# Performance work log

Hardware: AMD Instinct MI355X
Metric: run time of the kernel (lower is better)

The kernel has to match this reference:

```python
import jax, jax.numpy as jnp
import numpy as np

N_NODES = 1500
E = 48000
IN = 128
OUT = 32
HEADS = 4
EDIM = 16


def setup_inputs() -> dict:
    key = jax.random.key(0)
    ks = jax.random.split(key, 16)
    rn = lambda k, shape, s=0.1: jax.random.normal(k, shape, dtype=jnp.float32) * s
    return {
        "x": jax.random.normal(ks[0], (N_NODES, IN), dtype=jnp.float32),
        "edges": jax.random.randint(ks[1], (2, E), 0, N_NODES),
        "edge_feature": jax.random.normal(ks[2], (E, EDIM), dtype=jnp.float32),
        "W1": rn(ks[3], (IN, HEADS * OUT)),
        "att_src1": rn(ks[4], (HEADS, OUT)),
        "att_dst1": rn(ks[5], (HEADS, OUT)),
        "We": rn(ks[6], (EDIM, HEADS * OUT)),
        "att_e": rn(ks[7], (HEADS, OUT)),
        "b1": jnp.zeros((OUT,), jnp.float32),
        "W2": rn(ks[8], (OUT, HEADS * OUT)),
        "att_src2": rn(ks[9], (HEADS, OUT)),
        "att_dst2": rn(ks[10], (HEADS, OUT)),
        "b2": jnp.zeros((OUT,), jnp.float32),
        "fc1_w": rn(ks[11], (2 * OUT, 32)),
        "fc1_b": jnp.zeros((32,), jnp.float32),
        "fc2_w": rn(ks[12], (32, 2)),
        "fc2_b": jnp.zeros((2,), jnp.float32),
    }


def _gat(h, src, dst, n, a_src, a_dst, bias, extra_alpha=None):
    # h: [n, H, C] projected node features; edges j=src -> i=dst (PyG GATConv)
    alpha = (h * a_src).sum(-1)[src] + (h * a_dst).sum(-1)[dst]  # [Etot, H]
    if extra_alpha is not None:
        alpha = alpha + extra_alpha
    alpha = jax.nn.leaky_relu(alpha, negative_slope=0.2)
    m = jax.ops.segment_max(alpha, dst, num_segments=n)  # per-dst softmax (stable)
    e = jnp.exp(alpha - m[dst])
    s = jax.ops.segment_sum(e, dst, num_segments=n)
    w = e / s[dst]  # every node has a self loop -> denom > 0
    out = jax.ops.segment_sum(w[:, :, None] * h[src], dst, num_segments=n)  # [n, H, C]
    return out.mean(axis=1) + bias  # concat=False -> mean over heads


def reference(x, edges, edge_feature, W1, att_src1, att_dst1, We, att_e, b1,
              W2, att_src2, att_dst2, b2, fc1_w, fc1_b, fc2_w, fc2_b):
    n = x.shape[0]
    src0, dst0 = edges[0], edges[1]
    loop = jnp.arange(n, dtype=src0.dtype)
    src = jnp.concatenate([src0, loop])
    dst = jnp.concatenate([dst0, loop])
    # add_self_loops fill_value='mean': self-loop attr = mean of incoming edge attrs
    cnt = jax.ops.segment_sum(jnp.ones_like(dst0, dtype=jnp.float32), dst0, num_segments=n)
    loop_attr = jax.ops.segment_sum(edge_feature, dst0, num_segments=n) / jnp.maximum(cnt, 1.0)[:, None]
    ea = jnp.concatenate([edge_feature, loop_attr], axis=0)  # [E+n, EDIM]

    H, C = att_src1.shape
    # layer 1: GATConv with edge features
    h1 = (x @ W1).reshape(n, H, C)
    extra = ((ea @ We).reshape(-1, H, C) * att_e).sum(-1)  # [E+n, H]
    x1 = _gat(h1, src, dst, n, att_src1, att_dst1, b1, extra)  # [n, OUT]
    # layer 2: GATConv without edge features
    h2 = (x1 @ W2).reshape(n, H, C)
    x2 = _gat(h2, src, dst, n, att_src2, att_dst2, b2)  # [n, OUT]

    # per-edge gather-concat into a (n^2, 2*OUT) buffer; rows >= E stay zero,
    # exactly as the original Python loop leaves them
    pair = jnp.concatenate([x2[src0], x2[dst0]], axis=1)  # [E, 2*OUT]
    x_edges = jnp.zeros((n * n, 2 * C), dtype=x2.dtype).at[jnp.arange(src0.shape[0])].set(pair)
    hcls = jax.nn.relu(x_edges @ fc1_w + fc1_b)
    return jax.nn.softmax(hcls @ fc2_w + fc2_b, axis=1)
```

## Files before the change

kernel.cpp:

```cpp
#include <hip/hip_runtime.h>
#include <cmath>

#define N_NODES 1500
#define NE 48000
#define ETOT (NE + N_NODES)
#define IN_DIM 128
#define OUT_DIM 32
#define HEADS 4
#define HC 128
#define EDIM 16
#define CH 128

__global__ void k_init(int* deg, int* fillc, float* sumattr) {
    int gid = blockIdx.x * blockDim.x + threadIdx.x;
    if (gid < N_NODES) { deg[gid] = 0; fillc[gid] = 0; }
    if (gid < N_NODES * EDIM) sumattr[gid] = 0.f;
}

__global__ void k_deg_attr(const int* __restrict__ dst, const float* __restrict__ ef,
                           int* deg, float* sumattr) {
    int gid = blockIdx.x * blockDim.x + threadIdx.x;
    if (gid >= NE * EDIM) return;
    int e = gid >> 4, k = gid & 15;
    int d = dst[e];
    atomicAdd(&sumattr[d * EDIM + k], ef[gid]);
    if (k == 0) atomicAdd(&deg[d], 1);
}

__global__ void k_scan(const int* __restrict__ deg, int* __restrict__ off) {
    __shared__ int part[512];
    int t = threadIdx.x;
    int base = t * 3;
    int d0 = (base     < N_NODES) ? deg[base] + 1     : 0;
    int d1 = (base + 1 < N_NODES) ? deg[base + 1] + 1 : 0;
    int d2 = (base + 2 < N_NODES) ? deg[base + 2] + 1 : 0;
    int sum = d0 + d1 + d2;
    part[t] = sum;
    __syncthreads();
    for (int o = 1; o < 512; o <<= 1) {
        int v = (t >= o) ? part[t - o] : 0;
        __syncthreads();
        part[t] += v;
        __syncthreads();
    }
    int excl = part[t] - sum;
    if (base     <= N_NODES) off[base]     = excl;
    if (base + 1 <= N_NODES) off[base + 1] = excl + d0;
    if (base + 2 <= N_NODES) off[base + 2] = excl + d0 + d1;
}

__global__ void k_scatter(const int* __restrict__ src, const int* __restrict__ dst,
                          const int* __restrict__ off, int* fillc,
                          int* __restrict__ csr_src, int* __restrict__ csr_eid) {
    int e = blockIdx.x * blockDim.x + threadIdx.x;
    if (e >= ETOT) return;
    int s, d;
    if (e < NE) { s = src[e]; d = dst[e]; } else { s = d = e - NE; }
    int pos = atomicAdd(&fillc[d], 1);
    int idx = off[d] + pos;
    csr_src[idx] = s;
    csr_eid[idx] = e;
}

__global__ void k_extra(const float* __restrict__ ef, const float* __restrict__ We,
                        const float* __restrict__ att_e, const float* __restrict__ sumattr,
                        const int* __restrict__ deg, float* __restrict__ extra) {
    __shared__ float P[EDIM * HEADS];
    int t = threadIdx.x;
    if (t < EDIM * HEADS) {
        int k = t >> 2, hh = t & 3;
        float a = 0.f;
        #pragma unroll
        for (int c = 0; c < OUT_DIM; ++c)
            a = fmaf(We[k * HC + hh * OUT_DIM + c], att_e[hh * OUT_DIM + c], a);
        P[t] = a;
    }
    __syncthreads();
    int gid = blockIdx.x * blockDim.x + t;
    if (gid >= ETOT * HEADS) return;
    int e = gid >> 2, hh = gid & 3;
    float a = 0.f;
    if (e < NE) {
        #pragma unroll
        for (int k = 0; k < EDIM; ++k) a = fmaf(ef[e * EDIM + k], P[k * 4 + hh], a);
    } else {
        int i = e - NE;
        float inv = 1.0f / fmaxf((float)deg[i], 1.0f);
        #pragma unroll
        for (int k = 0; k < EDIM; ++k) a = fmaf(sumattr[i * EDIM + k] * inv, P[k * 4 + hh], a);
    }
    extra[gid] = a;
}

__global__ void k_proj1(const float* __restrict__ xin, const float* __restrict__ W,
                        const float* __restrict__ a_src, const float* __restrict__ a_dst,
                        float* __restrict__ h, float* __restrict__ asrc, float* __restrict__ adst) {
    __shared__ float xs[4][IN_DIM];
    int i0 = blockIdx.x * 4, t = threadIdx.x;
    #pragma unroll
    for (int r = 0; r < 4; ++r) xs[r][t] = xin[(i0 + r) * IN_DIM + t];
    __syncthreads();
    float acc0 = 0.f, acc1 = 0.f, acc2 = 0.f, acc3 = 0.f;
    for (int k = 0; k < IN_DIM; ++k) {
        float w = W[k * HC + t];
        acc0 = fmaf(xs[0][k], w, acc0);
        acc1 = fmaf(xs[1][k], w, acc1);
        acc2 = fmaf(xs[2][k], w, acc2);
        acc3 = fmaf(xs[3][k], w, acc3);
    }
    float as = a_src[t], ad = a_dst[t];
    int hh = t >> 5, c = t & 31;
    float accs[4] = {acc0, acc1, acc2, acc3};
    #pragma unroll
    for (int r = 0; r < 4; ++r) {
        h[(i0 + r) * HC + t] = accs[r];
        float ps = accs[r] * as, pd = accs[r] * ad;
        #pragma unroll
        for (int o = 16; o >= 1; o >>= 1) {
            ps += __shfl_down(ps, o, 32);
            pd += __shfl_down(pd, o, 32);
        }
        if (c == 0) { asrc[(i0 + r) * 4 + hh] = ps; adst[(i0 + r) * 4 + hh] = pd; }
    }
}

template <int MODE>
__global__ void k_gat(const float* __restrict__ h, const float* __restrict__ asrc,
                      const float* __restrict__ adst, const float* __restrict__ extra,
                      const int* __restrict__ off, const int* __restrict__ csr_src,
                      const int* __restrict__ csr_eid, const float* __restrict__ bias,
                      const float* __restrict__ Wn, const float* __restrict__ a_s2,
                      const float* __restrict__ a_d2,
                      float* __restrict__ h2, float* __restrict__ asrc2,
                      float* __restrict__ adst2, float* __restrict__ uv) {
    __shared__ int   sns[CH];
    __shared__ float sal[CH * HEADS];
    __shared__ float red[HC];
    __shared__ float xrow[OUT_DIM];
    int i = blockIdx.x, t = threadIdx.x;
    int hh = t >> 5, c = t & 31;
    float4 ad4 = *(const float4*)&adst[i * 4];
    int beg = off[i], end = off[i + 1];
    float m = -INFINITY, s = 0.f, acc = 0.f;
    for (int pos = beg; pos < end; pos += CH) {
        int cnt = min(CH, end - pos);
        __syncthreads();
        if (t < cnt) {
            int j = pos + t;
            int sn = csr_src[j];
            sns[t] = sn;
            float4 a4 = *(const float4*)&asrc[sn * 4];
            float ax = a4.x + ad4.x, ay = a4.y + ad4.y, az = a4.z + ad4.z, aw = a4.w + ad4.w;
            if (MODE == 1) {
                float4 e4 = *(const float4*)&extra[csr_eid[j] * 4];
                ax += e4.x; ay += e4.y; az += e4.z; aw += e4.w;
            }
            ax = ax > 0.f ? ax : 0.2f * ax;
            ay = ay > 0.f ? ay : 0.2f * ay;
            az = az > 0.f ? az : 0.2f * az;
            aw = aw > 0.f ? aw : 0.2f * aw;
            *(float4*)&sal[t * 4] = make_float4(ax, ay, az, aw);
        }
        __syncthreads();
        float cm = -INFINITY;
        for (int q = c; q < cnt; q += 32) cm = fmaxf(cm, sal[q * 4 + hh]);
        #pragma unroll
        for (int o = 16; o >= 1; o >>= 1) cm = fmaxf(cm, __shfl_down(cm, o, 32));
        cm = __shfl(cm, 0, 32);
        float mn = fmaxf(m, cm);
        float r = __expf(m - mn);
        float cs = 0.f;
        for (int q = c; q < cnt; q += 32) {
            float w = __expf(sal[q * 4 + hh] - mn);
            sal[q * 4 + hh] = w;
            cs += w;
        }
        #pragma unroll
        for (int o = 16; o >= 1; o >>= 1) cs += __shfl_down(cs, o, 32);
        cs = __shfl(cs, 0, 32);
        s = s * r + cs;
        acc *= r;
        m = mn;
        for (int jj = 0; jj < cnt; ++jj)
            acc = fmaf(sal[jj * 4 + hh], h[sns[jj] * HC + t], acc);
    }
    red[t] = acc / s;
    __syncthreads();
    if (t < OUT_DIM)
        xrow[t] = 0.25f * (red[t] + red[t + 32] + red[t + 64] + red[t + 96]) + bias[t];
    __syncthreads();
    if (MODE == 1) {
        float a2 = 0.f;
        #pragma unroll
        for (int k = 0; k < OUT_DIM; ++k) a2 = fmaf(xrow[k], Wn[k * HC + t], a2);
        h2[i * HC + t] = a2;
        float ps = a2 * a_s2[t], pd = a2 * a_d2[t];
        #pragma unroll
        for (int o = 16; o >= 1; o >>= 1) {
            ps += __shfl_down(ps, o, 32);
            pd += __shfl_down(pd, o, 32);
        }
        if (c == 0) { asrc2[i * 4 + hh] = ps; adst2[i * 4 + hh] = pd; }
    } else {
        if (t < 64) {
            int j = t & 31, ro = (t >> 5) * 32;
            float a2 = 0.f;
            #pragma unroll
            for (int k = 0; k < OUT_DIM; ++k) a2 = fmaf(xrow[k], Wn[(ro + k) * 32 + j], a2);
            uv[i * 64 + t] = a2;
        }
    }
}

__global__ void k_fill(const float* __restrict__ fc1b, const float* __restrict__ fc2w,
                       const float* __restrict__ fc2b, float* __restrict__ out) {
    float l0 = fc2b[0], l1 = fc2b[1];
    #pragma unroll
    for (int j = 0; j < 32; ++j) {
        float a = fmaxf(fc1b[j], 0.f);
        l0 = fmaf(a, fc2w[2 * j], l0);
        l1 = fmaf(a, fc2w[2 * j + 1], l1);
    }
    float mx = fmaxf(l0, l1);
    float e0 = __expf(l0 - mx), e1 = __expf(l1 - mx);
    float inv = 1.f / (e0 + e1);
    float4 q = make_float4(e0 * inv, e1 * inv, e0 * inv, e1 * inv);
    int gid = blockIdx.x * blockDim.x + threadIdx.x;
    const int nfl4 = ((N_NODES * N_NODES - NE) * 2) / 4;
    if (gid < nfl4) ((float4*)(out + NE * 2))[gid] = q;
}

__global__ void k_edge_mlp(const int* __restrict__ src, const int* __restrict__ dst,
                           const float* __restrict__ uv,
                           const float* __restrict__ fc1b,
                           const float* __restrict__ fc2w, const float* __restrict__ fc2b,
                           float* __restrict__ out) {
    __shared__ float b1s[32], w2s[64], b2s[2];
    int t = threadIdx.x;
    if (t < 32) b1s[t] = fc1b[t];
    if (t < 64) w2s[t] = fc2w[t];
    if (t < 2)  b2s[t] = fc2b[t];
    __syncthreads();
    int e = blockIdx.x * 256 + t;
    if (e >= NE) return;
    int si = src[e], di = dst[e];
    const float4* up = (const float4*)&uv[si * 64];
    const float4* vp = (const float4*)&uv[di * 64 + 32];
    float l0 = b2s[0], l1 = b2s[1];
    #pragma unroll
    for (int q = 0; q < 8; ++q) {
        float4 u4 = up[q], v4 = vp[q];
        float a;
        a = fmaxf(u4.x + v4.x + b1s[4*q+0], 0.f); l0 = fmaf(a, w2s[8*q+0], l0); l1 = fmaf(a, w2s[8*q+1], l1);
        a = fmaxf(u4.y + v4.y + b1s[4*q+1], 0.f); l0 = fmaf(a, w2s[8*q+2], l0); l1 = fmaf(a, w2s[8*q+3], l1);
        a = fmaxf(u4.z + v4.z + b1s[4*q+2], 0.f); l0 = fmaf(a, w2s[8*q+4], l0); l1 = fmaf(a, w2s[8*q+5], l1);
        a = fmaxf(u4.w + v4.w + b1s[4*q+3], 0.f); l0 = fmaf(a, w2s[8*q+6], l0); l1 = fmaf(a, w2s[8*q+7], l1);
    }
    float mx = fmaxf(l0, l1);
    float e0 = __expf(l0 - mx), e1 = __expf(l1 - mx);
    float inv = 1.f / (e0 + e1);
    *(float2*)&out[2 * e] = make_float2(e0 * inv, e1 * inv);
}

extern "C" void kernel_launch(void* const* d_in, const int* in_sizes, int n_in,
                              void* d_out, int out_size, void* d_ws, size_t ws_size,
                              hipStream_t stream) {
    (void)in_sizes; (void)n_in; (void)out_size; (void)ws_size;
    const float* x    = (const float*)d_in[0];
    const int*  edges = (const int*)d_in[1];
    const float* ef   = (const float*)d_in[2];
    const float* W1   = (const float*)d_in[3];
    const float* as1  = (const float*)d_in[4];
    const float* ad1  = (const float*)d_in[5];
    const float* We   = (const float*)d_in[6];
    const float* ate  = (const float*)d_in[7];
    const float* b1   = (const float*)d_in[8];
    const float* W2   = (const float*)d_in[9];
    const float* as2  = (const float*)d_in[10];
    const float* ad2  = (const float*)d_in[11];
    const float* b2   = (const float*)d_in[12];
    const float* fc1w = (const float*)d_in[13];
    const float* fc1b = (const float*)d_in[14];
    const float* fc2w = (const float*)d_in[15];
    const float* fc2b = (const float*)d_in[16];
    const int* src = edges;
    const int* dst = edges + NE;
    float* out = (float*)d_out;

    char* w = (char*)d_ws;
    auto alloc = [&](size_t bytes) -> char* {
        char* p = w;
        w += (bytes + 255) & ~(size_t)255;
        return p;
    };
    float* h1      = (float*)alloc((size_t)N_NODES * HC * 4);
    float* asrc1   = (float*)alloc((size_t)N_NODES * HEADS * 4);
    float* adst1   = (float*)alloc((size_t)N_NODES * HEADS * 4);
    float* extra   = (float*)alloc((size_t)ETOT * HEADS * 4);
    float* sumattr = (float*)alloc((size_t)N_NODES * EDIM * 4);
    int*   deg     = (int*)  alloc((size_t)N_NODES * 4);
    int*   off     = (int*)  alloc((size_t)(N_NODES + 1) * 4);
    int*   fillc   = (int*)  alloc((size_t)N_NODES * 4);
    int*   csr_src = (int*)  alloc((size_t)ETOT * 4);
    int*   csr_eid = (int*)  alloc((size_t)ETOT * 4);
    float* h2      = (float*)alloc((size_t)N_NODES * HC * 4);
    float* asrc2   = (float*)alloc((size_t)N_NODES * HEADS * 4);
    float* adst2   = (float*)alloc((size_t)N_NODES * HEADS * 4);
    float* uv      = (float*)alloc((size_t)N_NODES * 64 * 4);

    const int B = 256;
    k_init<<<(N_NODES * EDIM + B - 1) / B, B, 0, stream>>>(deg, fillc, sumattr);
    k_deg_attr<<<(NE * EDIM + B - 1) / B, B, 0, stream>>>(dst, ef, deg, sumattr);
    k_scan<<<1, 512, 0, stream>>>(deg, off);
    k_scatter<<<(ETOT + B - 1) / B, B, 0, stream>>>(src, dst, off, fillc, csr_src, csr_eid);
    k_extra<<<(ETOT * HEADS + B - 1) / B, B, 0, stream>>>(ef, We, ate, sumattr, deg, extra);
    k_proj1<<<N_NODES / 4, HC, 0, stream>>>(x, W1, as1, ad1, h1, asrc1, adst1);
    k_gat<1><<<N_NODES, HC, 0, stream>>>(h1, asrc1, adst1, extra, off, csr_src, csr_eid, b1,
                                         W2, as2, ad2, h2, asrc2, adst2, nullptr);
    k_gat<2><<<N_NODES, HC, 0, stream>>>(h2, asrc2, adst2, nullptr, off, csr_src, csr_eid, b2,
                                         fc1w, nullptr, nullptr, nullptr, nullptr, nullptr, uv);
    k_fill<<<((((N_NODES * N_NODES - NE) * 2) / 4) + B - 1) / B, B, 0, stream>>>(fc1b, fc2w, fc2b, out);
    k_edge_mlp<<<(NE + B - 1) / B, B, 0, stream>>>(src, dst, uv, fc1b, fc2w, fc2b, out);
}
```

Before: 157.9 us.

## Fuse all GAT pipeline stages into one persistent kernel with grid barriers

Ten separate launches (init, degree/attribute accumulation, scan, CSR scatter, edge-attention term, projection, two GAT layers, output fill, edge MLP) become one persistent kernel of 256 blocks × 256 threads. The phases are separated by a software grid barrier built on an atomic counter and sleep polling. The aim is to remove per-launch overhead and idle gaps between small kernels. The edge-feature attention term is also split so per-edge work overlaps the zeroing phase. In exchange, each GAT phase uses only 256 blocks looping over nodes with half the threads idle, and the large output fill has less parallelism. The barrier also relies on every block being co-resident.

Result: slower. 374.8 us (+137.4%).

```diff
diff --git a/kernel.cpp b/kernel.cpp
--- a/kernel.cpp
+++ b/kernel.cpp
@@ -9,141 +9,38 @@
 #define HEADS 4
 #define HC 128
 #define EDIM 16
-#define CH 128
-
-__global__ void k_init(int* deg, int* fillc, float* sumattr) {
-    int gid = blockIdx.x * blockDim.x + threadIdx.x;
-    if (gid < N_NODES) { deg[gid] = 0; fillc[gid] = 0; }
-    if (gid < N_NODES * EDIM) sumattr[gid] = 0.f;
+#define NBLK 256
+#define NTHR 256
+#define GSZ (NBLK * NTHR)
+
+__device__ __forceinline__ void gsync(int* bar, int goal) {
+    __syncthreads();
+    if (threadIdx.x == 0) {
+        __threadfence();
+        atomicAdd(bar, 1);
+        while (atomicAdd(bar, 0) < goal) __builtin_amdgcn_s_sleep(8);
+        __threadfence();
+    }
+    __syncthreads();
 }
 
-__global__ void k_deg_attr(const int* __restrict__ dst, const float* __restrict__ ef,
-                           int* deg, float* sumattr) {
-    int gid = blockIdx.x * blockDim.x + threadIdx.x;
-    if (gid >= NE * EDIM) return;
-    int e = gid >> 4, k = gid & 15;
-    int d = dst[e];
-    atomicAdd(&sumattr[d * EDIM + k], ef[gid]);
-    if (k == 0) atomicAdd(&deg[d], 1);
-}
-
-__global__ void k_scan(const int* __restrict__ deg, int* __restrict__ off) {
-    __shared__ int part[512];
+template <int MODE>
+__device__ __forceinline__ void gat_one(
+        int i, const float* __restrict__ h, const float* __restrict__ asrc,
+        const float* __restrict__ adst, const float* __restrict__ extra,
+        const int* __restrict__ off, const int* __restrict__ csr_src,
+        const int* __restrict__ csr_eid, const float* __restrict__ bias,
+        const float* __restrict__ Wn, const float* __restrict__ a_s2,
+        const float* __restrict__ a_d2, float* h2, float* asrc2, float* adst2,
+        float* uv, int* sns, float* sal, float* red, float* xrow)
+{
     int t = threadIdx.x;
-    int base = t * 3;
-    int d0 = (base     < N_NODES) ? deg[base] + 1     : 0;
-    int d1 = (base + 1 < N_NODES) ? deg[base + 1] + 1 : 0;
-    int d2 = (base + 2 < N_NODES) ? deg[base + 2] + 1 : 0;
-    int sum = d0 + d1 + d2;
-    part[t] = sum;
-    __syncthreads();
-    for (int o = 1; o < 512; o <<= 1) {
-        int v = (t >= o) ? part[t - o] : 0;
-        __syncthreads();
-        part[t] += v;
-        __syncthreads();
-    }
-    int excl = part[t] - sum;
-    if (base     <= N_NODES) off[base]     = excl;
-    if (base + 1 <= N_NODES) off[base + 1] = excl + d0;
-    if (base + 2 <= N_NODES) off[base + 2] = excl + d0 + d1;
-}
-
-__global__ void k_scatter(const int* __restrict__ src, const int* __restrict__ dst,
-                          const int* __restrict__ off, int* fillc,
-                          int* __restrict__ csr_src, int* __restrict__ csr_eid) {
-    int e = blockIdx.x * blockDim.x + threadIdx.x;
-    if (e >= ETOT) return;
-    int s, d;
-    if (e < NE) { s = src[e]; d = dst[e]; } else { s = d = e - NE; }
-    int pos = atomicAdd(&fillc[d], 1);
-    int idx = off[d] + pos;
-    csr_src[idx] = s;
-    csr_eid[idx] = e;
-}
-
-__global__ void k_extra(const float* __restrict__ ef, const float* __restrict__ We,
-                        const float* __restrict__ att_e, const float* __restrict__ sumattr,
-                        const int* __restrict__ deg, float* __restrict__ extra) {
-    __shared__ float P[EDIM * HEADS];
-    int t = threadIdx.x;
-    if (t < EDIM * HEADS) {
-        int k = t >> 2, hh = t & 3;
-        float a = 0.f;
-        #pragma unroll
-        for (int c = 0; c < OUT_DIM; ++c)
-            a = fmaf(We[k * HC + hh * OUT_DIM + c], att_e[hh * OUT_DIM + c], a);
-        P[t] = a;
-    }
-    __syncthreads();
-    int gid = blockIdx.x * blockDim.x + t;
-    if (gid >= ETOT * HEADS) return;
-    int e = gid >> 2, hh = gid & 3;
-    float a = 0.f;
-    if (e < NE) {
-        #pragma unroll
-        for (int k = 0; k < EDIM; ++k) a = fmaf(ef[e * EDIM + k], P[k * 4 + hh], a);
-    } else {
-        int i = e - NE;
-        float inv = 1.0f / fmaxf((float)deg[i], 1.0f);
-        #pragma unroll
-        for (int k = 0; k < EDIM; ++k) a = fmaf(sumattr[i * EDIM + k] * inv, P[k * 4 + hh], a);
-    }
-    extra[gid] = a;
-}
-
-__global__ void k_proj1(const float* __restrict__ xin, const float* __restrict__ W,
-                        const float* __restrict__ a_src, const float* __restrict__ a_dst,
-                        float* __restrict__ h, float* __restrict__ asrc, float* __restrict__ adst) {
-    __shared__ float xs[4][IN_DIM];
-    int i0 = blockIdx.x * 4, t = threadIdx.x;
-    #pragma unroll
-    for (int r = 0; r < 4; ++r) xs[r][t] = xin[(i0 + r) * IN_DIM + t];
-    __syncthreads();
-    float acc0 = 0.f, acc1 = 0.f, acc2 = 0.f, acc3 = 0.f;
-    for (int k = 0; k < IN_DIM; ++k) {
-        float w = W[k * HC + t];
-        acc0 = fmaf(xs[0][k], w, acc0);
-        acc1 = fmaf(xs[1][k], w, acc1);
-        acc2 = fmaf(xs[2][k], w, acc2);
-        acc3 = fmaf(xs[3][k], w, acc3);
-    }
-    float as = a_src[t], ad = a_dst[t];
-    int hh = t >> 5, c = t & 31;
-    float accs[4] = {acc0, acc1, acc2, acc3};
-    #pragma unroll
-    for (int r = 0; r < 4; ++r) {
-        h[(i0 + r) * HC + t] = accs[r];
-        float ps = accs[r] * as, pd = accs[r] * ad;
-        #pragma unroll
-        for (int o = 16; o >= 1; o >>= 1) {
-            ps += __shfl_down(ps, o, 32);
-            pd += __shfl_down(pd, o, 32);
-        }
-        if (c == 0) { asrc[(i0 + r) * 4 + hh] = ps; adst[(i0 + r) * 4 + hh] = pd; }
-    }
-}
-
-template <int MODE>
-__global__ void k_gat(const float* __restrict__ h, const float* __restrict__ asrc,
-                      const float* __restrict__ adst, const float* __restrict__ extra,
-                      const int* __restrict__ off, const int* __restrict__ csr_src,
-                      const int* __restrict__ csr_eid, const float* __restrict__ bias,
-                      const float* __restrict__ Wn, const float* __restrict__ a_s2,
-                      const float* __restrict__ a_d2,
-                      float* __restrict__ h2, float* __restrict__ asrc2,
-                      float* __restrict__ adst2, float* __restrict__ uv) {
-    __shared__ int   sns[CH];
-    __shared__ float sal[CH * HEADS];
-    __shared__ float red[HC];
-    __shared__ float xrow[OUT_DIM];
-    int i = blockIdx.x, t = threadIdx.x;
-    int hh = t >> 5, c = t & 31;
+    int beg = off[i], end = off[i + 1];
     float4 ad4 = *(const float4*)&adst[i * 4];
-    int beg = off[i], end = off[i + 1];
+    int hh = (t & 127) >> 5, c = t & 31;
     float m = -INFINITY, s = 0.f, acc = 0.f;
-    for (int pos = beg; pos < end; pos += CH) {
-        int cnt = min(CH, end - pos);
+    for (int pos = beg; pos < end; pos += 256) {
+        int cnt = min(256, end - pos);
         __syncthreads();
         if (t < cnt) {
             int j = pos + t;
@@ -159,48 +56,49 @@
             ay = ay > 0.f ? ay : 0.2f * ay;
             az = az > 0.f ? az : 0.2f * az;
             aw = aw > 0.f ? aw : 0.2f * aw;
-            *(float4*)&sal[t * 4] = make_float4(ax, ay, az, aw);
+            ((float4*)sal)[t] = make_float4(ax, ay, az, aw);
         }
         __syncthreads();
-        float cm = -INFINITY;
-        for (int q = c; q < cnt; q += 32) cm = fmaxf(cm, sal[q * 4 + hh]);
-        #pragma unroll
-        for (int o = 16; o >= 1; o >>= 1) cm = fmaxf(cm, __shfl_down(cm, o, 32));
-        cm = __shfl(cm, 0, 32);
-        float mn = fmaxf(m, cm);
-        float r = __expf(m - mn);
-        float cs = 0.f;
-        for (int q = c; q < cnt; q += 32) {
-            float w = __expf(sal[q * 4 + hh] - mn);
-            sal[q * 4 + hh] = w;
-            cs += w;
-        }
-        #pragma unroll
-        for (int o = 16; o >= 1; o >>= 1) cs += __shfl_down(cs, o, 32);
-        cs = __shfl(cs, 0, 32);
-        s = s * r + cs;
-        acc *= r;
-        m = mn;
-        for (int jj = 0; jj < cnt; ++jj)
-            acc = fmaf(sal[jj * 4 + hh], h[sns[jj] * HC + t], acc);
-    }
-    red[t] = acc / s;
+        if (t < 128) {
+            float cm = -INFINITY;
+            for (int q = c; q < cnt; q += 32) cm = fmaxf(cm, sal[q * 4 + hh]);
+            #pragma unroll
+            for (int o = 16; o >= 1; o >>= 1) cm = fmaxf(cm, __shfl_down(cm, o, 32));
+            cm = __shfl(cm, 0, 32);
+            float mn = fmaxf(m, cm);
+            float r = __expf(m - mn);
+            float cs = 0.f;
+            for (int q = c; q < cnt; q += 32) {
+                float w = __expf(sal[q * 4 + hh] - mn);
+                sal[q * 4 + hh] = w;
+                cs += w;
+            }
+            #pragma unroll
+            for (int o = 16; o >= 1; o >>= 1) cs += __shfl_down(cs, o, 32);
+            cs = __shfl(cs, 0, 32);
+            s = s * r + cs;
+            acc *= r;
+            m = mn;
+            for (int jj = 0; jj < cnt; ++jj)
+                acc = fmaf(sal[jj * 4 + hh], h[sns[jj] * HC + t], acc);
+        }
+    }
+    if (t < 128) red[t] = acc / s;
     __syncthreads();
     if (t < OUT_DIM)
         xrow[t] = 0.25f * (red[t] + red[t + 32] + red[t + 64] + red[t + 96]) + bias[t];
     __syncthreads();
     if (MODE == 1) {
-        float a2 = 0.f;
-        #pragma unroll
-        for (int k = 0; k < OUT_DIM; ++k) a2 = fmaf(xrow[k], Wn[k * HC + t], a2);
-        h2[i * HC + t] = a2;
-        float ps = a2 * a_s2[t], pd = a2 * a_d2[t];
-        #pragma unroll
-        for (int o = 16; o >= 1; o >>= 1) {
-            ps += __shfl_down(ps, o, 32);
-            pd += __shfl_down(pd, o, 32);
-        }
-        if (c == 0) { asrc2[i * 4 + hh] = ps; adst2[i * 4 + hh] = pd; }
+        if (t < 128) {
+            float a2 = 0.f;
+            #pragma unroll
+            for (int k = 0; k < OUT_DIM; ++k) a2 = fmaf(xrow[k], Wn[k * HC + t], a2);
+            h2[i * HC + t] = a2;
+            float ps = a2 * a_s2[t], pd = a2 * a_d2[t];
+            #pragma unroll
+            for (int o = 16; o >= 1; o >>= 1) { ps += __shfl_down(ps, o, 32); pd += __shfl_down(pd, o, 32); }
+            if (c == 0) { asrc2[i * 4 + hh] = ps; adst2[i * 4 + hh] = pd; }
+        }
     } else {
         if (t < 64) {
             int j = t & 31, ro = (t >> 5) * 32;
@@ -210,56 +108,183 @@
             uv[i * 64 + t] = a2;
         }
     }
+    __syncthreads();
 }
 
-__global__ void k_fill(const float* __restrict__ fc1b, const float* __restrict__ fc2w,
-                       const float* __restrict__ fc2b, float* __restrict__ out) {
-    float l0 = fc2b[0], l1 = fc2b[1];
-    #pragma unroll
-    for (int j = 0; j < 32; ++j) {
-        float a = fmaxf(fc1b[j], 0.f);
-        l0 = fmaf(a, fc2w[2 * j], l0);
-        l1 = fmaf(a, fc2w[2 * j + 1], l1);
-    }
-    float mx = fmaxf(l0, l1);
-    float e0 = __expf(l0 - mx), e1 = __expf(l1 - mx);
-    float inv = 1.f / (e0 + e1);
-    float4 q = make_float4(e0 * inv, e1 * inv, e0 * inv, e1 * inv);
-    int gid = blockIdx.x * blockDim.x + threadIdx.x;
-    const int nfl4 = ((N_NODES * N_NODES - NE) * 2) / 4;
-    if (gid < nfl4) ((float4*)(out + NE * 2))[gid] = q;
-}
-
-__global__ void k_edge_mlp(const int* __restrict__ src, const int* __restrict__ dst,
-                           const float* __restrict__ uv,
-                           const float* __restrict__ fc1b,
-                           const float* __restrict__ fc2w, const float* __restrict__ fc2b,
-                           float* __restrict__ out) {
-    __shared__ float b1s[32], w2s[64], b2s[2];
-    int t = threadIdx.x;
-    if (t < 32) b1s[t] = fc1b[t];
-    if (t < 64) w2s[t] = fc2w[t];
-    if (t < 2)  b2s[t] = fc2b[t];
-    __syncthreads();
-    int e = blockIdx.x * 256 + t;
-    if (e >= NE) return;
-    int si = src[e], di = dst[e];
-    const float4* up = (const float4*)&uv[si * 64];
-    const float4* vp = (const float4*)&uv[di * 64 + 32];
-    float l0 = b2s[0], l1 = b2s[1];
-    #pragma unroll
-    for (int q = 0; q < 8; ++q) {
-        float4 u4 = up[q], v4 = vp[q];
-        float a;
-        a = fmaxf(u4.x + v4.x + b1s[4*q+0], 0.f); l0 = fmaf(a, w2s[8*q+0], l0); l1 = fmaf(a, w2s[8*q+1], l1);
-        a = fmaxf(u4.y + v4.y + b1s[4*q+1], 0.f); l0 = fmaf(a, w2s[8*q+2], l0); l1 = fmaf(a, w2s[8*q+3], l1);
-        a = fmaxf(u4.z + v4.z + b1s[4*q+2], 0.f); l0 = fmaf(a, w2s[8*q+4], l0); l1 = fmaf(a, w2s[8*q+5], l1);
-        a = fmaxf(u4.w + v4.w + b1s[4*q+3], 0.f); l0 = fmaf(a, w2s[8*q+6], l0); l1 = fmaf(a, w2s[8*q+7], l1);
-    }
-    float mx = fmaxf(l0, l1);
-    float e0 = __expf(l0 - mx), e1 = __expf(l1 - mx);
-    float inv = 1.f / (e0 + e1);
-    *(float2*)&out[2 * e] = make_float2(e0 * inv, e1 * inv);
+__global__ __launch_bounds__(NTHR, 1) void k_mega(
+    const float* __restrict__ x, const int* __restrict__ edges,
+    const float* __restrict__ ef,
+    const float* __restrict__ W1, const float* __restrict__ as1, const float* __restrict__ ad1,
+    const float* __restrict__ We, const float* __restrict__ ate,
+    const float* __restrict__ b1,
+    const float* __restrict__ W2, const float* __restrict__ as2, const float* __restrict__ ad2,
+    const float* __restrict__ b2,
+    const float* __restrict__ fc1w, const float* __restrict__ fc1b,
+    const float* __restrict__ fc2w, const float* __restrict__ fc2b,
+    float* __restrict__ out,
+    float* h1, float* asrc1, float* adst1, float* extra, float* sumattr,
+    int* deg, int* off, int* fillc, int* csr_src, int* csr_eid,
+    float* h2, float* asrc2, float* adst2, float* uv, int* bar)
+{
+    const int t = threadIdx.x;
+    const int b = blockIdx.x;
+    const int gtid = b * NTHR + t;
+    const int* src = edges;
+    const int* dst = edges + NE;
+
+    __shared__ float P[EDIM * HEADS];
+    __shared__ float xs[6 * IN_DIM];
+    __shared__ int   part[256];
+    __shared__ int   sns[256];
+    __shared__ float sal[256 * HEADS];
+    __shared__ float red[HC];
+    __shared__ float xrow[OUT_DIM];
+
+    if (t < EDIM * HEADS) {
+        int k = t >> 2, hh = t & 3;
+        float a = 0.f;
+        #pragma unroll
+        for (int c = 0; c < OUT_DIM; ++c)
+            a = fmaf(We[k * HC + hh * OUT_DIM + c], ate[hh * OUT_DIM + c], a);
+        P[t] = a;
+    }
+    if (gtid < N_NODES) { deg[gtid] = 0; fillc[gtid] = 0; }
+    for (int idx = gtid; idx < N_NODES * EDIM; idx += GSZ) sumattr[idx] = 0.f;
+    {
+        float l0 = fc2b[0], l1 = fc2b[1];
+        #pragma unroll
+        for (int j = 0; j < 32; ++j) {
+            float a = fmaxf(fc1b[j], 0.f);
+            l0 = fmaf(a, fc2w[2 * j], l0);
+            l1 = fmaf(a, fc2w[2 * j + 1], l1);
+        }
+        float mx = fmaxf(l0, l1);
+        float e0 = __expf(l0 - mx), e1 = __expf(l1 - mx);
+        float inv = 1.f / (e0 + e1);
+        float4 q = make_float4(e0 * inv, e1 * inv, e0 * inv, e1 * inv);
+        float4* o4 = (float4*)(out + NE * 2);
+        const int nfl4 = ((N_NODES * N_NODES - NE) * 2) / 4;
+        for (int idx = gtid; idx < nfl4; idx += GSZ) o4[idx] = q;
+    }
+    __syncthreads();
+    for (int idx = gtid; idx < NE * HEADS; idx += GSZ) {
+        int e = idx >> 2, hh = idx & 3;
+        float a = 0.f;
+        #pragma unroll
+        for (int k = 0; k < EDIM; ++k) a = fmaf(ef[e * EDIM + k], P[k * 4 + hh], a);
+        extra[idx] = a;
+    }
+    gsync(bar, NBLK * 1);
+
+    if (gtid < NE) {
+        int d = dst[gtid];
+        atomicAdd(&deg[d], 1);
+        #pragma unroll
+        for (int k = 0; k < EDIM; ++k)
+            atomicAdd(&sumattr[d * EDIM + k], ef[gtid * EDIM + k]);
+    }
+    if (b < 250) {
+        int i0 = 6 * b;
+        for (int idx = t; idx < 6 * IN_DIM; idx += NTHR) xs[idx] = x[i0 * IN_DIM + idx];
+        __syncthreads();
+        int col = t & 127, g = t >> 7;
+        float a0 = 0.f, a1 = 0.f, a2 = 0.f;
+        for (int k = 0; k < IN_DIM; ++k) {
+            float w = W1[k * HC + col];
+            a0 = fmaf(xs[(g * 3 + 0) * IN_DIM + k], w, a0);
+            a1 = fmaf(xs[(g * 3 + 1) * IN_DIM + k], w, a1);
+            a2 = fmaf(xs[(g * 3 + 2) * IN_DIM + k], w, a2);
+        }
+        float as = as1[col], ad = ad1[col];
+        int hh = col >> 5, c = col & 31;
+        float av[3] = {a0, a1, a2};
+        #pragma unroll
+        for (int r = 0; r < 3; ++r) {
+            int node = i0 + g * 3 + r;
+            h1[node * HC + col] = av[r];
+            float ps = av[r] * as, pd = av[r] * ad;
+            #pragma unroll
+            for (int o = 16; o >= 1; o >>= 1) { ps += __shfl_down(ps, o, 32); pd += __shfl_down(pd, o, 32); }
+            if (c == 0) { asrc1[node * 4 + hh] = ps; adst1[node * 4 + hh] = pd; }
+        }
+    }
+    gsync(bar, NBLK * 2);
+
+    if (b == 0) {
+        int l[6];
+        int sum = 0;
+        if (t < 250) {
+            #pragma unroll
+            for (int j = 0; j < 6; ++j) { l[j] = sum; sum += deg[t * 6 + j] + 1; }
+        }
+        part[t] = sum;
+        __syncthreads();
+        for (int o = 1; o < 256; o <<= 1) {
+            int v = (t >= o) ? part[t - o] : 0;
+            __syncthreads();
+            part[t] += v;
+            __syncthreads();
+        }
+        if (t < 250) {
+            int excl = part[t] - sum;
+            #pragma unroll
+            for (int j = 0; j < 6; ++j) off[t * 6 + j] = excl + l[j];
+            if (t == 249) off[N_NODES] = excl + sum;
+        }
+    } else {
+        int gidx = gtid - NTHR;
+        if (gidx < N_NODES * HEADS) {
+            int i = gidx >> 2, hh = gidx & 3;
+            float inv = 1.f / fmaxf((float)deg[i], 1.f);
+            float a = 0.f;
+            #pragma unroll
+            for (int k = 0; k < EDIM; ++k) a = fmaf(sumattr[i * EDIM + k] * inv, P[k * 4 + hh], a);
+            extra[(NE + i) * 4 + hh] = a;
+        }
+    }
+    gsync(bar, NBLK * 3);
+
+    if (gtid < ETOT) {
+        int e = gtid, s_, d_;
+        if (e < NE) { s_ = src[e]; d_ = dst[e]; } else { s_ = d_ = e - NE; }
+        int pos = atomicAdd(&fillc[d_], 1);
+        int idx = off[d_] + pos;
+        csr_src[idx] = s_;
+        csr_eid[idx] = e;
+    }
+    gsync(bar, NBLK * 4);
+
+    for (int i = b; i < N_NODES; i += NBLK)
+        gat_one<1>(i, h1, asrc1, adst1, extra, off, csr_src, csr_eid, b1,
+                   W2, as2, ad2, h2, asrc2, adst2, nullptr, sns, sal, red, xrow);
+    gsync(bar, NBLK * 5);
+
+    for (int i = b; i < N_NODES; i += NBLK)
+        gat_one<2>(i, h2, asrc2, adst2, nullptr, off, csr_src, csr_eid, b2,
+                   fc1w, nullptr, nullptr, nullptr, nullptr, nullptr, uv,
+                   sns, sal, red, xrow);
+    gsync(bar, NBLK * 6);
+
+    if (gtid < NE) {
+        int e = gtid;
+        int si = src[e], di = dst[e];
+        const float4* up = (const float4*)&uv[si * 64];
+        const float4* vp = (const float4*)&uv[di * 64 + 32];
+        float l0 = fc2b[0], l1 = fc2b[1];
+        #pragma unroll
+        for (int q = 0; q < 8; ++q) {
+            float4 u4 = up[q], v4 = vp[q];
+            float a;
+            a = fmaxf(u4.x + v4.x + fc1b[4*q+0], 0.f); l0 = fmaf(a, fc2w[8*q+0], l0); l1 = fmaf(a, fc2w[8*q+1], l1);
+            a = fmaxf(u4.y + v4.y + fc1b[4*q+1], 0.f); l0 = fmaf(a, fc2w[8*q+2], l0); l1 = fmaf(a, fc2w[8*q+3], l1);
+            a = fmaxf(u4.z + v4.z + fc1b[4*q+2], 0.f); l0 = fmaf(a, fc2w[8*q+4], l0); l1 = fmaf(a, fc2w[8*q+5], l1);
+            a = fmaxf(u4.w + v4.w + fc1b[4*q+3], 0.f); l0 = fmaf(a, fc2w[8*q+6], l0); l1 = fmaf(a, fc2w[8*q+7], l1);
+        }
+        float mx = fmaxf(l0, l1);
+        float e0 = __expf(l0 - mx), e1 = __expf(l1 - mx);
+        float inv = 1.f / (e0 + e1);
+        *(float2*)&out[2 * e] = make_float2(e0 * inv, e1 * inv);
+    }
 }
 
 extern "C" void kernel_launch(void* const* d_in, const int* in_sizes, int n_in,
@@ -283,8 +308,6 @@
     const float* fc1b = (const float*)d_in[14];
     const float* fc2w = (const float*)d_in[15];
     const float* fc2b = (const float*)d_in[16];
-    const int* src = edges;
-    const int* dst = edges + NE;
     float* out = (float*)d_out;
 
     char* w = (char*)d_ws;
@@ -307,18 +330,12 @@
     float* asrc2   = (float*)alloc((size_t)N_NODES * HEADS * 4);
     float* adst2   = (float*)alloc((size_t)N_NODES * HEADS * 4);
     float* uv      = (float*)alloc((size_t)N_NODES * 64 * 4);
-
-    const int B = 256;
-    k_init<<<(N_NODES * EDIM + B - 1) / B, B, 0, stream>>>(deg, fillc, sumattr);
-    k_deg_attr<<<(NE * EDIM + B - 1) / B, B, 0, stream>>>(dst, ef, deg, sumattr);
-    k_scan<<<1, 512, 0, stream>>>(deg, off);
-    k_scatter<<<(ETOT + B - 1) / B, B, 0, stream>>>(src, dst, off, fillc, csr_src, csr_eid);
-    k_extra<<<(ETOT * HEADS + B - 1) / B, B, 0, stream>>>(ef, We, ate, sumattr, deg, extra);
-    k_proj1<<<N_NODES / 4, HC, 0, stream>>>(x, W1, as1, ad1, h1, asrc1, adst1);
-    k_gat<1><<<N_NODES, HC, 0, stream>>>(h1, asrc1, adst1, extra, off, csr_src, csr_eid, b1,
-                                         W2, as2, ad2, h2, asrc2, adst2, nullptr);
-    k_gat<2><<<N_NODES, HC, 0, stream>>>(h2, asrc2, adst2, nullptr, off, csr_src, csr_eid, b2,
-                                         fc1w, nullptr, nullptr, nullptr, nullptr, nullptr, uv);
-    k_fill<<<((((N_NODES * N_NODES - NE) * 2) / 4) + B - 1) / B, B, 0, stream>>>(fc1b, fc2w, fc2b, out);
-    k_edge_mlp<<<(NE + B - 1) / B, B, 0, stream>>>(src, dst, uv, fc1b, fc2w, fc2b, out);
+    int*   bar     = (int*)  alloc(256);
+
+    hipMemsetAsync(bar, 0, sizeof(int), stream);
+    k_mega<<<NBLK, NTHR, 0, stream>>>(
+        x, edges, ef, W1, as1, ad1, We, ate, b1, W2, as2, ad2, b2,
+        fc1w, fc1b, fc2w, fc2b, out,
+        h1, asrc1, adst1, extra, sumattr, deg, off, fillc, csr_src, csr_eid,
+        h2, asrc2, adst2, uv, bar);
 }
```
